# Kernel tuning notes

Hardware: AMD Instinct MI355X
Metric: run time of the kernel (lower is better)

Reference implementation:

```python
import jax, jax.numpy as jnp
import numpy as np

B, S, D, H = 4, 2048, 256, 8  # batch, seq (context=target), hidden_dim, n_heads


def setup_inputs() -> dict:
    key = jax.random.key(0)
    ks = jax.random.split(key, 12)
    sd = 1.0 / np.sqrt(D)          # torch Linear default init scale (uniform bound)
    sdo = 1.0 / np.sqrt(H * D)
    inp = {
        "k": jax.random.normal(ks[0], (B, S, D), jnp.float32),
        "v": jax.random.normal(ks[1], (B, S, D), jnp.float32),
        "q": jax.random.normal(ks[2], (B, S, D), jnp.float32),
        # Per-head projection weights, stacked over heads. Stored so y = x @ W + b.
        "Wk": jax.random.uniform(ks[3], (H, D, D), jnp.float32, -sd, sd),
        "bk": jax.random.uniform(ks[4], (H, D), jnp.float32, -sd, sd),
        "Wv": jax.random.uniform(ks[5], (H, D, D), jnp.float32, -sd, sd),
        "bv": jax.random.uniform(ks[6], (H, D), jnp.float32, -sd, sd),
        "Wq": jax.random.uniform(ks[7], (H, D, D), jnp.float32, -sd, sd),
        "bq": jax.random.uniform(ks[8], (H, D), jnp.float32, -sd, sd),
        # Final mixing Linear: input is heads interleaved as (hidden, head) flattened,
        # i.e. input index = hid * H + head (torch stack(dim=-1).view order).
        "Wo": jax.random.uniform(ks[9], (H * D, D), jnp.float32, -sdo, sdo),
        "bo": jax.random.uniform(ks[10], (D,), jnp.float32, -sdo, sdo),
    }
    return inp


def reference(k, v, q, Wk, bk, Wv, bv, Wq, bq, Wo, bo):
    # Per-head linear projections (batched over heads instead of a Python loop)
    k_ = jnp.einsum('bmd,hde->bhme', k, Wk) + bk[None, :, None, :]  # [B,H,S,D]
    v_ = jnp.einsum('bmd,hde->bhme', v, Wv) + bv[None, :, None, :]
    q_ = jnp.einsum('bnd,hde->bhne', q, Wq) + bq[None, :, None, :]
    scale = jnp.asarray(np.sqrt(D), k.dtype)
    # dot attention: scores[b,h,n,m] = <q_n, k_m> / sqrt(D); softmax over keys m
    scores = jnp.einsum('bhnd,bhmd->bhnm', q_, k_) / scale
    w = jax.nn.softmax(scores, axis=-1)
    rep = jnp.einsum('bhnm,bhmd->bhnd', w, v_)  # [B,H,S,D]
    # torch: stack(heads, dim=-1) -> [B,S,D,H], then view -> [B,S,D*H] (hid-major)
    outs = rep.transpose(0, 2, 3, 1).reshape(rep.shape[0], rep.shape[2], -1)
    return outs @ Wo + bo
```

## Files before the change

### kernel.cpp

```cpp
#include <hip/hip_runtime.h>

#define BB 4
#define SS 2048
#define DD 256
#define HH 8

typedef unsigned short u16;
typedef __attribute__((ext_vector_type(8))) short bf16x8;
typedef __attribute__((ext_vector_type(4))) float f32x4;
typedef __attribute__((ext_vector_type(16))) float f32x16;
typedef __attribute__((ext_vector_type(4))) short s16x4;

__device__ __forceinline__ f32x4 MFMA(bf16x8 a, bf16x8 b, f32x4 c) {
    return __builtin_amdgcn_mfma_f32_16x16x32_bf16(a, b, c, 0, 0, 0);
}
__device__ __forceinline__ f32x16 MFMA32(bf16x8 a, bf16x8 b, f32x16 c) {
    return __builtin_amdgcn_mfma_f32_32x32x16_bf16(a, b, c, 0, 0, 0);
}

__device__ __forceinline__ u16 f2bf_rtn(float x) {
    unsigned u = __float_as_uint(x);
    u += 0x7FFFu + ((u >> 16) & 1u);
    return (u16)(u >> 16);
}
__device__ __forceinline__ float bf2f(u16 h) {
    return __uint_as_float(((unsigned)h) << 16);
}
__device__ __forceinline__ void split2(float x, u16 &hi, u16 &lo) {
    hi = f2bf_rtn(x);
    lo = f2bf_rtn(x - bf2f(hi));
}

__device__ __forceinline__ void gl_lds16(const u16* g, u16* l) {
    __builtin_amdgcn_global_load_lds(
        (const __attribute__((address_space(1))) unsigned int*)(g),
        (__attribute__((address_space(3))) unsigned int*)(l), 16, 0, 0);
}

__global__ void prep_a(const float* __restrict__ x, u16* __restrict__ hi) {
    int r = blockIdx.x;
    int d = threadIdx.x;
    hi[(size_t)r * 256 + d] = f2bf_rtn(x[(size_t)r * 256 + d]);
}

__global__ void prep_w(const float* __restrict__ W, u16* __restrict__ Whi,
                       u16* __restrict__ Wlo) {
    int n = blockIdx.x;
    int h = n >> 8, e = n & 255;
    int d = threadIdx.x;
    float x = W[((size_t)h * 256 + d) * 256 + e];
    u16 hi, lo; split2(x, hi, lo);
    Whi[(size_t)n * 256 + d] = hi;
    Wlo[(size_t)n * 256 + d] = lo;
}

__global__ void prep_wo(const float* __restrict__ W, u16* __restrict__ Whi,
                        u16* __restrict__ Wlo) {
    int n = blockIdx.x;
    for (int k = threadIdx.x; k < 2048; k += 256) {
        int d = k & 255, h = k >> 8;
        float x = W[((size_t)(d * 8 + h)) * 256 + n];
        u16 hi, lo; split2(x, hi, lo);
        Whi[(size_t)n * 2048 + k] = hi;
        Wlo[(size_t)n * 2048 + k] = lo;
    }
}

template<int MODE, int AMODE, int TERMS, int BN>
__global__ __launch_bounds__(512, 2) void gemm_split(
    const u16* __restrict__ Ahi, const u16* __restrict__ Alo,
    const u16* __restrict__ Bhi, const u16* __restrict__ Blo,
    const float* __restrict__ bias,
    u16* __restrict__ Ohi,
    float* __restrict__ Of,
    int M, int N, int K, float scale)
{
    constexpr int WN = (BN == 128) ? 4 : 2;
    constexpr int WM = 8 / WN;
    constexpr int MSUB = (128 / WM) / 16;
    constexpr int NSUB = (BN / WN) / 16;
    constexpr int NPL = (TERMS == 3) ? 4 : (TERMS == 2) ? 3 : 2;

    __shared__ u16 lds[2 * NPL * 4096];

    const int tid = threadIdx.x;
    const int lane = tid & 63, wave = tid >> 6;
    const int wm = wave / WN, wn = wave % WN;
    const int m0 = blockIdx.y * 128, n0 = blockIdx.x * BN;

    f32x4 acc[MSUB][NSUB];
#pragma unroll
    for (int i = 0; i < MSUB; ++i)
#pragma unroll
        for (int j = 0; j < NSUB; ++j) acc[i][j] = {0.f, 0.f, 0.f, 0.f};

    const int rho = tid >> 2;
    const int Xs = (tid & 3) << 3;
    const int ldsW = wave * 512;

#define G_ISSUE(k0v, p)                                                         \
    {   u16* Bse = lds + (p) * (NPL * 4096);                                    \
        size_t ga;                                                              \
        if (AMODE == 0)                                                         \
            ga = (size_t)(m0 + rho) * K + (k0v) + Xs;                           \
        else                                                                    \
            ga = ((size_t)((m0 >> 11) * 8 + ((k0v) >> 8)) * SS                  \
                  + (m0 & 2047) + rho) * DD + ((k0v) & 255) + Xs;               \
        gl_lds16(Ahi + ga, Bse + ldsW);                                         \
        if (TERMS == 3) gl_lds16(Alo + ga, Bse + 3 * 4096 + ldsW);              \
        if (BN == 128 || tid < 256) {                                           \
            size_t gb = (size_t)(n0 + rho) * K + (k0v) + Xs;                    \
            gl_lds16(Bhi + gb, Bse + 1 * 4096 + ldsW);                          \
            if (TERMS >= 2) gl_lds16(Blo + gb, Bse + 2 * 4096 + ldsW);          \
        }                                                                       \
    }

    const int NK = K >> 5;
    G_ISSUE(0, 0);
    __syncthreads();

    for (int kt = 0; kt < NK; ++kt) {
        if (kt < NK - 1) G_ISSUE((kt + 1) << 5, (kt + 1) & 1);

        const u16* Bse = lds + (kt & 1) * (NPL * 4096);
        const int g8 = (lane >> 4) << 3;
        const int rA = wm * (128 / WM), rB = wn * (BN / WN);
        bf16x8 bh[NSUB], bl[NSUB];
#pragma unroll
        for (int ns = 0; ns < NSUB; ++ns) {
            const int rb = rB + ns * 16 + (lane & 15);
            bh[ns] = *(const bf16x8*)(Bse + 1 * 4096 + rb * 32 + g8);
            if (TERMS >= 2) bl[ns] = *(const bf16x8*)(Bse + 2 * 4096 + rb * 32 + g8);
        }
#pragma unroll
        for (int ms = 0; ms < MSUB; ++ms) {
            const int ra = rA + ms * 16 + (lane & 15);
            bf16x8 ah = *(const bf16x8*)(Bse + ra * 32 + g8);
            bf16x8 al;
            if (TERMS == 3) al = *(const bf16x8*)(Bse + 3 * 4096 + ra * 32 + g8);
#pragma unroll
            for (int ns = 0; ns < NSUB; ++ns) {
                acc[ms][ns] = MFMA(ah, bh[ns], acc[ms][ns]);
                if (TERMS == 3) acc[ms][ns] = MFMA(al, bh[ns], acc[ms][ns]);
                if (TERMS >= 2) acc[ms][ns] = MFMA(ah, bl[ns], acc[ms][ns]);
            }
        }
        __syncthreads();
    }
#undef G_ISSUE

#pragma unroll
    for (int ms = 0; ms < MSUB; ++ms)
#pragma unroll
        for (int ns = 0; ns < NSUB; ++ns)
#pragma unroll
            for (int r = 0; r < 4; ++r) {
                int row = m0 + wm * (128 / WM) + ms * 16 + (lane >> 4) * 4 + r;
                int col = n0 + wn * (BN / WN) + ns * 16 + (lane & 15);
                float v = (acc[ms][ns][r] + bias[col]) * scale;
                if (MODE == 2) {
                    Of[(size_t)row * N + col] = v;
                } else {
                    int b = row >> 11, s = row & 2047, hh = col >> 8, e = col & 255;
                    size_t idx;
                    if (MODE == 0)
                        idx = ((size_t)(b * HH + hh) * SS + s) * DD + e;
                    else
                        idx = ((size_t)(b * HH + hh) * DD + e) * SS + s;
                    Ohi[idx] = f2bf_rtn(v);
                }
            }
}

__global__ __launch_bounds__(256, 2) void attn_kernel(
    const u16* __restrict__ Qhi,
    const u16* __restrict__ Khi,
    const u16* __restrict__ Vhi,
    u16* __restrict__ Rhi, u16* __restrict__ Rlo)
{
    __shared__ u16 lK[2][32][256];
    __shared__ u16 lV[2][256][32];

    const int tid = threadIdx.x, lane = tid & 63, wave = tid >> 6;
    const int qc = lane & 31, g2 = lane >> 5;
    const int wg = ((blockIdx.x & 7) << 6) + (blockIdx.x >> 3);
    const int bh = wg >> 4;
    const int qt = wg & 15;
    const size_t base = (size_t)bh * SS * DD;
    const int q0w = qt * 128 + wave * 32;

    bf16x8 qB[16];
#pragma unroll
    for (int ks = 0; ks < 16; ++ks)
        qB[ks] = *(const bf16x8*)(Qhi + base + (size_t)(q0w + qc) * DD + ks * 16 + g2 * 8);

    int koff[4], voff[4];
#pragma unroll
    for (int q = 0; q < 4; ++q) {
        const int s = wave * 256 + q * 64 + lane;
        const int kr = s >> 5, kX = s & 31;
        const int kap = (kr & 0x13) | ((kr & 4) << 1) | ((kr & 8) >> 1);
        koff[q] = kap * DD + ((kX ^ kr) << 3);
        const int ve = s >> 2, vXs = s & 3;
        voff[q] = ve * SS + (((vXs ^ ((ve >> 3) & 3))) << 3);
    }

    float l_part = 0.f;
    f32x16 acc[8];
#pragma unroll
    for (int ec = 0; ec < 8; ++ec) acc[ec] = {};

#define ISSUE(tt, p)                                                            \
    {   const u16* Kg = Khi + base + (size_t)(tt) * 32 * DD;                    \
        const u16* Vg = Vhi + base + (size_t)(tt) * 32;                         \
        u16* Kb = &lK[p][0][0]; u16* Vb = &lV[p][0][0];                         \
        _Pragma("unroll")                                                       \
        for (int q = 0; q < 4; ++q) {                                           \
            gl_lds16(Kg + koff[q], Kb + (wave * 4 + q) * 512);                  \
            gl_lds16(Vg + voff[q], Vb + (wave * 4 + q) * 512);                  \
        }                                                                       \
    }

    ISSUE(0, 0);
    __syncthreads();

    for (int t = 0; t < 64; ++t) {
        if (t < 63) ISSUE(t + 1, (t + 1) & 1);

        const u16* Kb = &lK[t & 1][0][0];
        const u16* Vb = &lV[t & 1][0][0];

        f32x16 sa = {}, sb = {};
        __builtin_amdgcn_s_setprio(1);
#pragma unroll
        for (int ks = 0; ks < 8; ++ks) {
            bf16x8 ka = *(const bf16x8*)(Kb + qc * DD + (((2 * ks + g2) ^ qc) << 3));
            bf16x8 kb2 = *(const bf16x8*)(Kb + qc * DD + (((2 * (ks + 8) + g2) ^ qc) << 3));
            sa = MFMA32(ka, qB[ks], sa);
            sb = MFMA32(kb2, qB[ks + 8], sb);
        }
        __builtin_amdgcn_s_setprio(0);

        f32x16 s = sa + sb;
#pragma unroll
        for (int n = 0; n < 16; ++n) s[n] = __builtin_amdgcn_exp2f(s[n] - 8.0f);
        float tl = 0.f;
#pragma unroll
        for (int n = 0; n < 16; ++n) tl += s[n];
        l_part += tl;

        bf16x8 p0, p1;
#pragma unroll
        for (int j = 0; j < 8; ++j) p0[j] = (short)f2bf_rtn(s[j]);
#pragma unroll
        for (int j = 0; j < 8; ++j) p1[j] = (short)f2bf_rtn(s[8 + j]);

        __builtin_amdgcn_s_setprio(1);
#pragma unroll
        for (int ec = 0; ec < 8; ++ec) {
            const int e = ec * 32 + qc;
            bf16x8 v0 = *(const bf16x8*)(Vb + e * 32 + (((g2 ^ ((e >> 3) & 3))) << 3));
            bf16x8 v1 = *(const bf16x8*)(Vb + e * 32 + ((((2 + g2) ^ ((e >> 3) & 3))) << 3));
            acc[ec] = MFMA32(v0, p0, acc[ec]);
            acc[ec] = MFMA32(v1, p1, acc[ec]);
        }
        __builtin_amdgcn_s_setprio(0);

        __syncthreads();
    }
#undef ISSUE

    float l = l_part + __shfl_xor(l_part, 32);
    float inv = 1.0f / l;
    const size_t rowbase = ((size_t)bh * SS + q0w + qc) * DD;
#pragma unroll
    for (int ec = 0; ec < 8; ++ec)
#pragma unroll
        for (int rr = 0; rr < 4; ++rr) {
            const int e0 = ec * 32 + 8 * rr + 4 * g2;
            s16x4 hv, lv;
#pragma unroll
            for (int j = 0; j < 4; ++j) {
                u16 h2, l2; split2(acc[ec][4 * rr + j] * inv, h2, l2);
                hv[j] = (short)h2; lv[j] = (short)l2;
            }
            *(s16x4*)(Rhi + rowbase + e0) = hv;
            *(s16x4*)(Rlo + rowbase + e0) = lv;
        }
}

extern "C" void kernel_launch(void* const* d_in, const int* in_sizes, int n_in,
                              void* d_out, int out_size, void* d_ws, size_t ws_size,
                              hipStream_t stream)
{
    (void)in_sizes; (void)n_in; (void)out_size; (void)ws_size;
    const float* k_in = (const float*)d_in[0];
    const float* v_in = (const float*)d_in[1];
    const float* q_in = (const float*)d_in[2];
    const float* Wk   = (const float*)d_in[3];
    const float* bk   = (const float*)d_in[4];
    const float* Wv   = (const float*)d_in[5];
    const float* bv   = (const float*)d_in[6];
    const float* Wq   = (const float*)d_in[7];
    const float* bq   = (const float*)d_in[8];
    const float* Wo   = (const float*)d_in[9];
    const float* bo   = (const float*)d_in[10];
    float* out = (float*)d_out;

    char* p = (char*)d_ws;
    const size_t MB = 1024 * 1024;
    u16* WqH = (u16*)(p + 0 * MB);
    u16* WqL = (u16*)(p + 1 * MB);
    u16* WkH = (u16*)(p + 2 * MB);
    u16* WkL = (u16*)(p + 3 * MB);
    u16* WvH = (u16*)(p + 4 * MB);
    u16* WvL = (u16*)(p + 5 * MB);
    u16* WoH = (u16*)(p + 6 * MB);
    u16* WoL = (u16*)(p + 7 * MB);
    const size_t PB = 32 * MB;
    u16* QH  = (u16*)(p + 8 * MB);
    u16* KH  = (u16*)(p + 8 * MB + 1 * PB);
    u16* VTH = (u16*)(p + 8 * MB + 2 * PB);
    u16* RH  = (u16*)(p + 8 * MB + 3 * PB);
    u16* RL  = (u16*)(p + 8 * MB + 4 * PB);
    u16* AqH = (u16*)(p + 168 * MB);
    u16* AkH = (u16*)(p + 172 * MB);
    u16* AvH = (u16*)(p + 176 * MB);

    prep_a<<<dim3(8192), dim3(256), 0, stream>>>(q_in, AqH);
    prep_a<<<dim3(8192), dim3(256), 0, stream>>>(k_in, AkH);
    prep_a<<<dim3(8192), dim3(256), 0, stream>>>(v_in, AvH);
    prep_w<<<dim3(2048), dim3(256), 0, stream>>>(Wq, WqH, WqL);
    prep_w<<<dim3(2048), dim3(256), 0, stream>>>(Wk, WkH, WkL);
    prep_w<<<dim3(2048), dim3(256), 0, stream>>>(Wv, WvH, WvL);
    prep_wo<<<dim3(256), dim3(256), 0, stream>>>(Wo, WoH, WoL);

    const float qscale = 1.4426950408889634f / 16.0f;
    gemm_split<0, 0, 1, 128><<<dim3(16, 64), dim3(512), 0, stream>>>(
        AqH, nullptr, WqH, WqL, bq, QH, nullptr, 8192, 2048, 256, qscale);
    gemm_split<0, 0, 1, 128><<<dim3(16, 64), dim3(512), 0, stream>>>(
        AkH, nullptr, WkH, WkL, bk, KH, nullptr, 8192, 2048, 256, 1.0f);
    gemm_split<1, 0, 2, 128><<<dim3(16, 64), dim3(512), 0, stream>>>(
        AvH, nullptr, WvH, WvL, bv, VTH, nullptr, 8192, 2048, 256, 1.0f);

    attn_kernel<<<dim3(512), dim3(256), 0, stream>>>(
        QH, KH, VTH, RH, RL);

    gemm_split<2, 2, 3, 64><<<dim3(4, 64), dim3(512), 0, stream>>>(
        RH, RL, WoH, WoL, bo, nullptr, out, 8192, 256, 2048, 1.0f);
}
```

Before: 325.1 us.

## Use 512-thread attention blocks with triple-buffered K/V and a single barrier

The attention kernel now runs 8 waves per block covering 256 queries, so each K/V tile staged in LDS is shared by twice as many queries and each thread issues fewer loads. K/V staging goes from double to triple buffering with a prefetch distance of two tiles. A manual vmcnt wait plus one s_barrier at the top of each iteration replaces the trailing __syncthreads. The goal is more reuse of LDS tiles and better overlap of global loads with MFMA work. The cost is only 256 blocks, which may leave part of the GPU underused, plus more LDS per block.

```diff
diff --git a/kernel.cpp b/kernel.cpp
--- a/kernel.cpp
+++ b/kernel.cpp
@@ -172,37 +172,37 @@
             }
 }
 
-__global__ __launch_bounds__(256, 2) void attn_kernel(
+__global__ __launch_bounds__(512, 2) void attn_kernel(
     const u16* __restrict__ Qhi,
     const u16* __restrict__ Khi,
     const u16* __restrict__ Vhi,
     u16* __restrict__ Rhi, u16* __restrict__ Rlo)
 {
-    __shared__ u16 lK[2][32][256];
-    __shared__ u16 lV[2][256][32];
+    __shared__ u16 lK[3][8192];
+    __shared__ u16 lV[3][8192];
 
     const int tid = threadIdx.x, lane = tid & 63, wave = tid >> 6;
     const int qc = lane & 31, g2 = lane >> 5;
-    const int wg = ((blockIdx.x & 7) << 6) + (blockIdx.x >> 3);
-    const int bh = wg >> 4;
-    const int qt = wg & 15;
+    const int wg = ((blockIdx.x & 7) << 5) + (blockIdx.x >> 3);
+    const int bh = wg >> 3;
+    const int qt = wg & 7;
     const size_t base = (size_t)bh * SS * DD;
-    const int q0w = qt * 128 + wave * 32;
+    const int q0w = qt * 256 + wave * 32;
 
     bf16x8 qB[16];
 #pragma unroll
     for (int ks = 0; ks < 16; ++ks)
         qB[ks] = *(const bf16x8*)(Qhi + base + (size_t)(q0w + qc) * DD + ks * 16 + g2 * 8);
 
-    int koff[4], voff[4];
-#pragma unroll
-    for (int q = 0; q < 4; ++q) {
-        const int s = wave * 256 + q * 64 + lane;
+    int koff[2], voff[2];
+#pragma unroll
+    for (int i = 0; i < 2; ++i) {
+        const int s = tid + i * 512;
         const int kr = s >> 5, kX = s & 31;
         const int kap = (kr & 0x13) | ((kr & 4) << 1) | ((kr & 8) >> 1);
-        koff[q] = kap * DD + ((kX ^ kr) << 3);
+        koff[i] = kap * DD + ((kX ^ kr) << 3);
         const int ve = s >> 2, vXs = s & 3;
-        voff[q] = ve * SS + (((vXs ^ ((ve >> 3) & 3))) << 3);
+        voff[i] = ve * SS + (((vXs ^ ((ve >> 3) & 3))) << 3);
     }
 
     float l_part = 0.f;
@@ -213,22 +213,27 @@
 #define ISSUE(tt, p)                                                            \
     {   const u16* Kg = Khi + base + (size_t)(tt) * 32 * DD;                    \
         const u16* Vg = Vhi + base + (size_t)(tt) * 32;                         \
-        u16* Kb = &lK[p][0][0]; u16* Vb = &lV[p][0][0];                         \
-        _Pragma("unroll")                                                       \
-        for (int q = 0; q < 4; ++q) {                                           \
-            gl_lds16(Kg + koff[q], Kb + (wave * 4 + q) * 512);                  \
-            gl_lds16(Vg + voff[q], Vb + (wave * 4 + q) * 512);                  \
-        }                                                                       \
+        u16* Kb = &lK[p][0]; u16* Vb = &lV[p][0];                               \
+        gl_lds16(Kg + koff[0], Kb + wave * 512);                                \
+        gl_lds16(Kg + koff[1], Kb + wave * 512 + 4096);                         \
+        gl_lds16(Vg + voff[0], Vb + wave * 512);                                \
+        gl_lds16(Vg + voff[1], Vb + wave * 512 + 4096);                         \
     }
 
     ISSUE(0, 0);
-    __syncthreads();
+    ISSUE(1, 1);
 
     for (int t = 0; t < 64; ++t) {
-        if (t < 63) ISSUE(t + 1, (t + 1) & 1);
-
-        const u16* Kb = &lK[t & 1][0][0];
-        const u16* Vb = &lV[t & 1][0][0];
+        if (t < 63) { asm volatile("s_waitcnt vmcnt(4)" ::: "memory"); }
+        else        { asm volatile("s_waitcnt vmcnt(0)" ::: "memory"); }
+        __builtin_amdgcn_sched_barrier(0);
+        __builtin_amdgcn_s_barrier();
+        __builtin_amdgcn_sched_barrier(0);
+
+        if (t + 2 < 64) ISSUE(t + 2, (t + 2) % 3);
+
+        const u16* Kb = &lK[t % 3][0];
+        const u16* Vb = &lV[t % 3][0];
 
         f32x16 sa = {}, sb = {};
         __builtin_amdgcn_s_setprio(1);
@@ -265,8 +270,6 @@
             acc[ec] = MFMA32(v1, p1, acc[ec]);
         }
         __builtin_amdgcn_s_setprio(0);
-
-        __syncthreads();
     }
 #undef ISSUE
 
@@ -343,7 +346,7 @@
     gemm_split<1, 0, 2, 128><<<dim3(16, 64), dim3(512), 0, stream>>>(
         AvH, nullptr, WvH, WvL, bv, VTH, nullptr, 8192, 2048, 256, 1.0f);
 
-    attn_kernel<<<dim3(512), dim3(256), 0, stream>>>(
+    attn_kernel<<<dim3(256), dim3(512), 0, stream>>>(
         QH, KH, VTH, RH, RL);
 
     gemm_split<2, 2, 3, 64><<<dim3(4, 64), dim3(512), 0, stream>>>(
```

New measurement: 313.8 us. 3.5% less time.
